# Kernel optimization log

Measured on AMD Instinct MI355X. Metric: run time of the kernel, lower is better.

The kernel has to match this reference:

```python
import jax, jax.numpy as jnp
import numpy as np

N, E, H, D, C, L = 20000, 320000, 8, 64, 512, 2  # nodes, edges, heads, head_dim, channels, layers


def layer_norm(x, g, b, eps=1e-5):
    mu = x.mean(-1, keepdims=True)
    var = ((x - mu) ** 2).mean(-1, keepdims=True)
    return (x - mu) / jnp.sqrt(var + eps) * g + b


def setup_inputs() -> dict:
    key = jax.random.key(0)
    ks = jax.random.split(key, 14)
    s = 0.02
    x = jax.random.normal(ks[0], (N, C), jnp.float32)
    edge_index = jax.random.randint(ks[1], (2, E), 0, N, jnp.int32)
    edge_type = jax.random.randint(ks[2], (E,), 0, 10, jnp.int32)
    edge_repre = jax.random.normal(ks[3], (E,), jnp.float32)
    # Per-layer TransformerConv params (query/key/value/skip linears, each with bias)
    Wq = jax.random.normal(ks[4], (L, C, C), jnp.float32) * s
    Wk = jax.random.normal(ks[5], (L, C, C), jnp.float32) * s
    Wv = jax.random.normal(ks[6], (L, C, C), jnp.float32) * s
    Ws = jax.random.normal(ks[7], (L, C, C), jnp.float32) * s
    bq = jnp.zeros((L, C), jnp.float32)
    bk = jnp.zeros((L, C), jnp.float32)
    bv = jnp.zeros((L, C), jnp.float32)
    bs = jnp.zeros((L, C), jnp.float32)
    # FFN + shared LayerNorm
    W1 = jax.random.normal(ks[8], (C, 2 * C), jnp.float32) * s
    b1 = jnp.zeros((2 * C,), jnp.float32)
    W2 = jax.random.normal(ks[9], (2 * C, C), jnp.float32) * s
    b2 = jnp.zeros((C,), jnp.float32)
    ln_g = jnp.ones((C,), jnp.float32)
    ln_b = jnp.zeros((C,), jnp.float32)
    return {"x": x, "edge_index": edge_index, "edge_type": edge_type, "edge_repre": edge_repre,
            "Wq": Wq, "bq": bq, "Wk": Wk, "bk": bk, "Wv": Wv, "bv": bv, "Ws": Ws, "bs": bs,
            "W1": W1, "b1": b1, "W2": W2, "b2": b2, "ln_g": ln_g, "ln_b": ln_b}


def reference(x, edge_index, edge_type, edge_repre, Wq, bq, Wk, bk, Wv, bv, Ws, bs, W1, b1, W2, b2, ln_g, ln_b):
    src, dst = edge_index[0], edge_index[1]  # messages flow src -> dst (PyG source_to_target)
    enc = x
    scale = 1.0 / jnp.sqrt(jnp.float32(D))
    for l in range(L):
        q = (x @ Wq[l] + bq[l]).reshape(N, H, D)
        k = (x @ Wk[l] + bk[l]).reshape(N, H, D)
        v = (x @ Wv[l] + bv[l]).reshape(N, H, D)
        # per-edge attention logits [E, H]
        a = (q[dst] * k[src]).sum(-1) * scale
        # segment softmax over edges sharing a destination node
        amax = jax.ops.segment_max(a, dst, num_segments=N)
        amax = jnp.where(jnp.isfinite(amax), amax, 0.0)
        e = jnp.exp(a - amax[dst])
        denom = jax.ops.segment_sum(e, dst, num_segments=N)
        alpha = e / (denom[dst] + 1e-16)
        # scatter-aggregate weighted values, concat heads
        agg = jax.ops.segment_sum(alpha[:, :, None] * v[src], dst, num_segments=N).reshape(N, C)
        # root/skip connection (beta=False) + module-level residual to enc_emb
        x = agg + (x @ Ws[l] + bs[l]) + enc
    x = layer_norm(x, ln_g, ln_b)
    x = (jax.nn.relu(x @ W1 + b1) @ W2 + b2) + x
    x = layer_norm(x, ln_g, ln_b)
    return x + enc
```

## Files before the change

### kernel.cpp

```cpp
#include <hip/hip_runtime.h>

typedef __attribute__((ext_vector_type(8))) short short8;
typedef __attribute__((ext_vector_type(4))) float f32x4;

__device__ __forceinline__ unsigned short f2b(float f){
  union { float f; unsigned u; } x; x.f = f;
  unsigned r = x.u + 0x7fffu + ((x.u >> 16) & 1u);
  return (unsigned short)(r >> 16);
}
__device__ __forceinline__ float b2f(unsigned short v){
  union { unsigned u; float f; } x; x.u = ((unsigned)v) << 16; return x.f;
}

__device__ __forceinline__ int pslot(int t){
  return (t & ~7) | ((t & 3) << 1) | ((t >> 2) & 1);
}

__device__ __forceinline__ unsigned char enc1(float v){
#if __has_builtin(__builtin_amdgcn_cvt_pk_fp8_f32)
  return (unsigned char)(__builtin_amdgcn_cvt_pk_fp8_f32(v, v, 0, false) & 0xff);
#else
  union{float f;unsigned u;}x; x.f=v;
  unsigned s = x.u >> 31;
  float av = fabsf(v);
  if (av >= 448.f) return (unsigned char)((s<<7)|0x7e);
  if (av < 0.0078125f){ unsigned d=(unsigned)(av*512.f+0.5f); return (unsigned char)((s<<7)|d); }
  unsigned q = x.u & 0x7fffffff;
  q = q + 0x7ffff + ((q>>20)&1);
  int e2 = (int)(q>>23) - 127;
  unsigned m3 = (q>>20)&7;
  if (e2 < -6){ unsigned d=(unsigned)(av*512.f+0.5f); return (unsigned char)((s<<7)|d); }
  return (unsigned char)((s<<7) | ((unsigned)(e2+7)<<3) | m3);
#endif
}
__device__ __forceinline__ unsigned pk4(float a,float b,float c,float d){
#if __has_builtin(__builtin_amdgcn_cvt_pk_fp8_f32)
  int v = __builtin_amdgcn_cvt_pk_fp8_f32(a, b, 0, false);
  v = __builtin_amdgcn_cvt_pk_fp8_f32(c, d, v, true);
  return (unsigned)v;
#else
  return (unsigned)enc1(a) | ((unsigned)enc1(b)<<8) | ((unsigned)enc1(c)<<16) | ((unsigned)enc1(d)<<24);
#endif
}
__device__ __forceinline__ void dec4(unsigned u, float* o){
#if __has_builtin(__builtin_amdgcn_cvt_pk_f32_fp8)
  auto lo = __builtin_amdgcn_cvt_pk_f32_fp8((int)u, false);
  auto hi = __builtin_amdgcn_cvt_pk_f32_fp8((int)u, true);
  o[0]=lo[0]; o[1]=lo[1]; o[2]=hi[0]; o[3]=hi[1];
#else
  #pragma unroll
  for (int j=0;j<4;j++){
    unsigned b = (u >> (8*j)) & 0xffu;
    unsigned s = b >> 7, ex = (b >> 3) & 15u, mn = b & 7u;
    union{unsigned u;float f;} x;
    x.u = ex ? ((s<<31)|((ex+120u)<<23)|(mn<<20)) : (s<<31);
    o[j] = x.f;
  }
#endif
}

__global__ void count_k(const int* __restrict__ dst, int* __restrict__ deg, int E){
  int e = blockIdx.x*256 + threadIdx.x;
  if (e < E) atomicAdd(&deg[dst[e]], 1);
}

__global__ void scan_k(const int* __restrict__ deg, int* __restrict__ rowstart,
                       int* __restrict__ cursor, int n)
{
  __shared__ int wsum[16];
  int tid = threadIdx.x, lane = tid & 63, wv = tid >> 6;
  int CH = (n + 1023) >> 10;
  int b0 = tid * CH; if (b0 > n) b0 = n;
  int bend = b0 + CH; if (bend > n) bend = n;
  int sum = 0;
  for (int i = b0; i < bend; ++i) sum += deg[i];
  int xs = sum;
  #pragma unroll
  for (int o=1;o<64;o<<=1){ int t = __shfl_up(xs, o, 64); if (lane >= o) xs += t; }
  if (lane == 63) wsum[wv] = xs;
  __syncthreads();
  if (tid < 16){
    int w = wsum[tid];
    #pragma unroll
    for (int o=1;o<16;o<<=1){ int t = __shfl_up(w, o, 64); if (tid >= o) w += t; }
    wsum[tid] = w;
  }
  __syncthreads();
  int off = (wv ? wsum[wv-1] : 0) + xs - sum;
  int run = off;
  for (int i = b0; i < bend; ++i){ rowstart[i] = run; cursor[i] = run; run += deg[i]; }
  if (b0 < n && bend == n) rowstart[n] = run;
  if (n == 0 && tid == 0) rowstart[0] = 0;
}

__global__ void fill_k(const int* __restrict__ src, const int* __restrict__ dst,
                       int* __restrict__ cursor, int* __restrict__ csrc, int E){
  int e = blockIdx.x*256 + threadIdx.x;
  if (e < E){
    int p = atomicAdd(&cursor[dst[e]], 1);
    csrc[p] = src[e];
  }
}

__global__ void transpose_all_k(const float* __restrict__ Wq, const float* __restrict__ Wk,
  const float* __restrict__ Wv, const float* __restrict__ Ws,
  const float* __restrict__ W1, const float* __restrict__ W2,
  unsigned char* __restrict__ wtqkvs8, unsigned char* __restrict__ wt1_8,
  unsigned char* __restrict__ wt2_8)
{
  int bid = blockIdx.x;
  const float* src; unsigned char* dst; int r, c, lb;
  if (bid < 1024){
    int j = bid >> 7;
    int l = j >> 2, w = j & 3;
    src = (w==0?Wq : w==1?Wk : w==2?Wv : Ws) + (size_t)l*512*512;
    dst = wtqkvs8 + ((size_t)l*2048 + (size_t)w*512)*512;
    r = 512; c = 512; lb = bid & 127;
  } else if (bid < 1280){ src = W1; dst = wt1_8; r = 512; c = 1024; lb = bid - 1024; }
  else { src = W2; dst = wt2_8; r = 1024; c = 512; lb = bid - 1280; }
  int idx = lb*256 + threadIdx.x;
  int o = idx % c;
  int i0 = (idx / c) << 3;
  float v[8];
  #pragma unroll
  for (int t=0;t<8;t++) v[t] = 64.f * src[(size_t)(i0+t)*c + o];
  unsigned lo = pk4(v[0],v[1],v[2],v[3]);
  unsigned hi = pk4(v[4],v[5],v[6],v[7]);
  *(unsigned long long*)&dst[(size_t)o*r + pslot(i0>>3)*8] =
      (unsigned long long)lo | ((unsigned long long)hi << 32);
}

__global__ void cvt8_k(const float* __restrict__ in, unsigned char* __restrict__ out8,
                       unsigned short* __restrict__ outb, size_t n){
  size_t i = ((size_t)blockIdx.x*256 + threadIdx.x)*8;
  if (i >= n) return;
  const float4* p = (const float4*)(in + i);
  float4 a0 = p[0], a1 = p[1];
  short8 vv;
  ((unsigned short*)&vv)[0] = f2b(a0.x); ((unsigned short*)&vv)[1] = f2b(a0.y);
  ((unsigned short*)&vv)[2] = f2b(a0.z); ((unsigned short*)&vv)[3] = f2b(a0.w);
  ((unsigned short*)&vv)[4] = f2b(a1.x); ((unsigned short*)&vv)[5] = f2b(a1.y);
  ((unsigned short*)&vv)[6] = f2b(a1.z); ((unsigned short*)&vv)[7] = f2b(a1.w);
  *(short8*)&outb[i] = vv;
  unsigned lo = pk4(a0.x,a0.y,a0.z,a0.w);
  unsigned hi = pk4(a1.x,a1.y,a1.z,a1.w);
  size_t op = (i & ~(size_t)511) | ((size_t)pslot((int)((i & 511) >> 3)) << 3);
  *(unsigned long long*)&out8[op] = (unsigned long long)lo | ((unsigned long long)hi<<32);
}

template<int MODE, int KC, int NN>
__global__ __launch_bounds__(256) void gemm8_k(
    const unsigned char* __restrict__ A8,
    const unsigned char* __restrict__ Bt8,
    int M,
    const float* __restrict__ bias0, const float* __restrict__ bias1,
    const float* __restrict__ bias2, const float* __restrict__ bias3,
    unsigned short* __restrict__ qb, unsigned short* __restrict__ skipb,
    unsigned char* __restrict__ outC,
    float* __restrict__ outF, const float* __restrict__ res)
{
  __shared__ __align__(16) unsigned char lA[128*128];
  __shared__ __align__(16) unsigned char lB[128*128];
  const int tid  = threadIdx.x;
  const int lane = tid & 63;
  const int wid  = tid >> 6;

  const int nwg = gridDim.x;
  int id = blockIdx.x;
  int q = nwg >> 3, r = nwg & 7;
  int xc = id & 7, yy = id >> 3;
  int swz = (xc < r ? xc*(q+1) : r*(q+1) + (xc-r)*q) + yy;
  const int bm = (swz / NN) * 128;
  const int bn = (swz % NN) * 128;
  const int wm = (wid >> 1) * 64;
  const int wn = (wid & 1) * 64;

  f32x4 acc[4][4];
  #pragma unroll
  for (int m=0;m<4;m++)
    #pragma unroll
    for (int n=0;n<4;n++) acc[m][n] = (f32x4)0.f;

  const int kq = lane >> 4;

  for (int kt = 0; kt < KC; kt += 128){
    #pragma unroll
    for (int it = 0; it < 4; ++it) {
      int chunk = it*256 + tid;
      int row = chunk >> 3;
      int cin = chunk & 7;
      int scol = (cin ^ (row & 7)) * 16;
      int ga = bm + row; if (ga >= M) ga = M - 1;
      __builtin_amdgcn_global_load_lds(
        (const __attribute__((address_space(1))) void*)(A8 + (size_t)ga*KC + kt + scol),
        (__attribute__((address_space(3))) void*)(&lA[(it*256 + (wid<<6))*16]),
        16, 0, 0);
      __builtin_amdgcn_global_load_lds(
        (const __attribute__((address_space(1))) void*)(Bt8 + (size_t)(bn + row)*KC + kt + scol),
        (__attribute__((address_space(3))) void*)(&lB[(it*256 + (wid<<6))*16]),
        16, 0, 0);
    }
    __syncthreads();
    #pragma unroll
    for (int S = 0; S < 2; ++S){
      ulonglong2 af[4], bfv[4];
      #pragma unroll
      for (int m=0;m<4;m++){
        int rr = wm + m*16 + (lane & 15);
        int c  = (S*4 + kq) ^ (rr & 7);
        af[m] = *(const ulonglong2*)&lA[rr*128 + c*16];
      }
      #pragma unroll
      for (int n=0;n<4;n++){
        int rr = wn + n*16 + (lane & 15);
        int c  = (S*4 + kq) ^ (rr & 7);
        bfv[n] = *(const ulonglong2*)&lB[rr*128 + c*16];
      }
      #pragma unroll
      for (int m=0;m<4;m++)
        #pragma unroll
        for (int n=0;n<4;n++){
          acc[m][n] = __builtin_amdgcn_mfma_f32_16x16x32_fp8_fp8(
              (long)af[m].x, (long)bfv[n].x, acc[m][n], 0,0,0);
          acc[m][n] = __builtin_amdgcn_mfma_f32_16x16x32_fp8_fp8(
              (long)af[m].y, (long)bfv[n].y, acc[m][n], 0,0,0);
        }
    }
    __syncthreads();
  }

  #pragma unroll
  for (int m=0;m<4;m++){
    int row0 = bm + wm + m*16 + ((lane >> 4) << 2);
    #pragma unroll
    for (int n=0;n<4;n++){
      int col = bn + wn + n*16 + (lane & 15);
      float bval;
      if (MODE == 0){
        bval = (col < 512) ? bias0[col]
             : (col < 1024) ? bias1[col-512]
             : (col < 1536) ? bias2[col-1024] : bias3[col-1536];
      } else {
        bval = bias0[col];
      }
      #pragma unroll
      for (int r4=0;r4<4;r4++){
        int row = row0 + r4;
        if (row < M){
          float v = acc[m][n][r4] * 0.015625f + bval;
          if (MODE == 0){
            if (col < 512)       qb[(size_t)row*512 + col] = f2b(v);
            else if (col < 1536) outC[(size_t)row*1024 + (col-512)] = enc1(v);
            else                 skipb[(size_t)row*512 + (col-1536)] = f2b(v);
          } else if (MODE == 1){
            v = fmaxf(v, 0.0f);
            int pc = (pslot(col >> 3) << 3) | (col & 7);
            outC[(size_t)row*1024 + pc] = enc1(v);
          } else {
            v += res[(size_t)row*512 + col];
            outF[(size_t)row*512 + col] = v;
          }
        }
      }
    }
  }
}

template<int OUT>
__global__ __launch_bounds__(256) void attn_k(
  const unsigned short* __restrict__ qb, const unsigned char* __restrict__ kv8,
  const unsigned short* __restrict__ skipb, const unsigned short* __restrict__ encb,
  const int* __restrict__ rowstart, const int* __restrict__ csrc,
  float* __restrict__ xout, unsigned char* __restrict__ xout8, int N)
{
  int n = blockIdx.x*4 + (threadIdx.x>>6);
  if (n >= N) return;
  int lane = threadIdx.x & 63;

  const short8 qv = *(const short8*)&qb[(size_t)n*512 + lane*8];
  size_t base = (size_t)n*512 + (size_t)lane*8;
  const short8 sv = *(const short8*)&skipb[base];
  const short8 ev = *(const short8*)&encb[base];
  float qf[8];
  #pragma unroll
  for (int j=0;j<8;j++) qf[j] = b2f(((const unsigned short*)&qv)[j]);

  float l = 0.f;
  float acc[8] = {0.f,0.f,0.f,0.f,0.f,0.f,0.f,0.f};
  int e = rowstart[n], e1 = rowstart[n+1];
  if (e < e1){
    int s0 = csrc[e];
    int s1 = (e+1 < e1) ? csrc[e+1] : s0;
    uint2 k0 = *(const uint2*)&kv8[(size_t)s0*1024 + lane*8];
    uint2 v0 = *(const uint2*)&kv8[(size_t)s0*1024 + 512 + lane*8];
    uint2 k1 = *(const uint2*)&kv8[(size_t)s1*1024 + lane*8];
    uint2 v1 = *(const uint2*)&kv8[(size_t)s1*1024 + 512 + lane*8];
    for (; e < e1; ++e){
      int s2 = (e+2 < e1) ? csrc[e+2] : s0;
      uint2 k2 = *(const uint2*)&kv8[(size_t)s2*1024 + lane*8];
      uint2 v2 = *(const uint2*)&kv8[(size_t)s2*1024 + 512 + lane*8];
      float kf[8]; dec4(k0.x, kf); dec4(k0.y, kf+4);
      float dot = 0.f;
      #pragma unroll
      for (int j=0;j<8;j++) dot += qf[j]*kf[j];
      dot += __shfl_xor(dot,1); dot += __shfl_xor(dot,2); dot += __shfl_xor(dot,4);
      float p = __expf(dot * 0.125f);
      l += p;
      float vf[8]; dec4(v0.x, vf); dec4(v0.y, vf+4);
      #pragma unroll
      for (int j=0;j<8;j++) acc[j] += p*vf[j];
      k0 = k1; v0 = v1; k1 = k2; v1 = v2;
    }
  }
  float inv = 1.f/(l + 1e-16f);
  float o[8];
  #pragma unroll
  for (int j=0;j<8;j++)
    o[j] = acc[j]*inv + b2f(((const unsigned short*)&sv)[j]) + b2f(((const unsigned short*)&ev)[j]);
  if (OUT == 0){
    unsigned lo = pk4(o[0],o[1],o[2],o[3]);
    unsigned hi = pk4(o[4],o[5],o[6],o[7]);
    size_t op = (size_t)n*512 + ((size_t)pslot(lane) << 3);
    *(unsigned long long*)&xout8[op] = (unsigned long long)lo | ((unsigned long long)hi<<32);
  } else {
    float4* po = (float4*)&xout[base];
    po[0] = make_float4(o[0],o[1],o[2],o[3]);
    po[1] = make_float4(o[4],o[5],o[6],o[7]);
  }
}

template<int MODE>
__global__ __launch_bounds__(256) void ln_k(const float* __restrict__ x,
  const float* __restrict__ g, const float* __restrict__ b,
  float* __restrict__ outF, unsigned char* __restrict__ out8,
  const float* __restrict__ addv, int N)
{
  int n = blockIdx.x*4 + (threadIdx.x>>6);
  if (n >= N) return;
  int lane = threadIdx.x & 63;
  size_t base = (size_t)n*512 + (size_t)lane*8;
  const float4* p = (const float4*)(x + base);
  float4 a0 = p[0], a1 = p[1];
  float v[8] = {a0.x,a0.y,a0.z,a0.w,a1.x,a1.y,a1.z,a1.w};
  float s=0.f, ss=0.f;
  #pragma unroll
  for (int j=0;j<8;j++){ s += v[j]; ss += v[j]*v[j]; }
  #pragma unroll
  for (int o=1;o<64;o<<=1){ s += __shfl_xor(s,o); ss += __shfl_xor(ss,o); }
  float mean = s * (1.f/512.f);
  float var  = ss * (1.f/512.f) - mean*mean;
  float rstd = rsqrtf(var + 1e-5f);
  float o[8];
  #pragma unroll
  for (int j=0;j<8;j++){
    int c = lane*8 + j;
    o[j] = (v[j]-mean)*rstd*g[c] + b[c];
  }
  if (MODE == 0){
    float4* po = (float4*)&outF[base];
    po[0] = make_float4(o[0],o[1],o[2],o[3]);
    po[1] = make_float4(o[4],o[5],o[6],o[7]);
    unsigned lo = pk4(o[0],o[1],o[2],o[3]);
    unsigned hi = pk4(o[4],o[5],o[6],o[7]);
    size_t op = (size_t)n*512 + ((size_t)pslot(lane) << 3);
    *(unsigned long long*)&out8[op] = (unsigned long long)lo | ((unsigned long long)hi<<32);
  } else {
    #pragma unroll
    for (int j=0;j<8;j++) outF[base+j] = o[j] + addv[base+j];
  }
}

extern "C" void kernel_launch(void* const* d_in, const int* in_sizes, int n_in,
                              void* d_out, int out_size, void* d_ws, size_t ws_size,
                              hipStream_t stream)
{
  const float* x0  = (const float*)d_in[0];
  const int*  eidx = (const int*)d_in[1];
  const float* Wq  = (const float*)d_in[4];
  const float* bq  = (const float*)d_in[5];
  const float* Wk  = (const float*)d_in[6];
  const float* bk  = (const float*)d_in[7];
  const float* Wv  = (const float*)d_in[8];
  const float* bv  = (const float*)d_in[9];
  const float* Wsk = (const float*)d_in[10];
  const float* bs  = (const float*)d_in[11];
  const float* W1  = (const float*)d_in[12];
  const float* b1  = (const float*)d_in[13];
  const float* W2  = (const float*)d_in[14];
  const float* b2  = (const float*)d_in[15];
  const float* lng = (const float*)d_in[16];
  const float* lnb = (const float*)d_in[17];

  const int N = in_sizes[0] / 512;
  const int E = in_sizes[1] / 2;
  const int* esrc = eidx;
  const int* edst = eidx + E;

  char* ws = (char*)d_ws;
  size_t off = 0;
  auto alloc = [&](size_t bytes)->char*{
    char* p = ws + off; off = (off + bytes + 255) & ~(size_t)255; return p;
  };
  unsigned char*  wtqkvs8 = (unsigned char*)alloc((size_t)2*2048*512);
  unsigned char*  wt1_8   = (unsigned char*)alloc((size_t)1024*512);
  unsigned char*  wt2_8   = (unsigned char*)alloc((size_t)512*1024);
  unsigned short* qb      = (unsigned short*)alloc((size_t)N*512*2);
  unsigned char*  kv8     = (unsigned char*)alloc((size_t)N*1024);
  float*          skip    = (float*)alloc((size_t)N*512*4);
  float*          xbuf    = (float*)alloc((size_t)N*512*4);
  unsigned char*  xb8     = (unsigned char*)alloc((size_t)N*512);
  unsigned short* encb    = (unsigned short*)alloc((size_t)N*512*2);
  unsigned short* skipb   = (unsigned short*)alloc((size_t)N*512*2);
  int* deg      = (int*)alloc((size_t)N*4);
  int* rowstart = (int*)alloc((size_t)(N+1)*4);
  int* cursor   = (int*)alloc((size_t)N*4);
  int* csrc     = (int*)alloc((size_t)E*4);
  unsigned char* t8 = (unsigned char*)qb;
  unsigned char* h8 = xb8;

  hipMemsetAsync(deg, 0, (size_t)N*4, stream);
  count_k<<<(E+255)/256, 256, 0, stream>>>(edst, deg, E);
  scan_k<<<1, 1024, 0, stream>>>(deg, rowstart, cursor, N);
  fill_k<<<(E+255)/256, 256, 0, stream>>>(esrc, edst, cursor, csrc, E);

  transpose_all_k<<<1536, 256, 0, stream>>>(Wq, Wk, Wv, Wsk, W1, W2, wtqkvs8, wt1_8, wt2_8);

  const int cvtBlocks = (int)(((size_t)N*512/8 + 255)/256);
  const int rowBlocks = (N + 3)/4;
  const int MB = (N + 127)/128;

  cvt8_k<<<cvtBlocks, 256, 0, stream>>>(x0, xb8, encb, (size_t)N*512);
  for (int l = 0; l < 2; ++l){
    gemm8_k<0,512,16><<<MB*16, 256, 0, stream>>>(xb8, wtqkvs8 + (size_t)l*2048*512, N,
        bq + l*512, bk + l*512, bv + l*512, bs + l*512, qb, skipb, kv8, nullptr, nullptr);
    if (l == 0)
      attn_k<0><<<rowBlocks, 256, 0, stream>>>(qb, kv8, skipb, encb, rowstart, csrc,
          nullptr, xb8, N);
    else
      attn_k<1><<<rowBlocks, 256, 0, stream>>>(qb, kv8, skipb, encb, rowstart, csrc,
          xbuf, nullptr, N);
  }

  ln_k<0><<<rowBlocks, 256, 0, stream>>>(xbuf, lng, lnb, skip, h8, nullptr, N);
  gemm8_k<1,512,8><<<MB*8, 256, 0, stream>>>(h8, wt1_8, N,
      b1, nullptr, nullptr, nullptr, nullptr, nullptr, t8, nullptr, nullptr);
  gemm8_k<2,1024,4><<<MB*4, 256, 0, stream>>>(t8, wt2_8, N,
      b2, nullptr, nullptr, nullptr, nullptr, nullptr, nullptr, xbuf, skip);
  ln_k<1><<<rowBlocks, 256, 0, stream>>>(xbuf, lng, lnb, (float*)d_out, nullptr, x0, N);
}
```

Baseline: 463.2 us.

## Fuse first LayerNorm into attention kernel and enlarge QKV GEMM M-tile

The second-layer attention kernel now computes the row LayerNorm itself and writes both the fp32 normalized activations and the fp8 copy. This removes a separate ln kernel launch and its round trip through global memory. The GEMM gains an MF template parameter, and the QKVS projection uses 256-row tiles so more reuse comes from each B tile. The trade-off is higher register and LDS use (more accumulators per wave), which may reduce occupancy.

```diff
diff --git a/kernel.cpp b/kernel.cpp
--- a/kernel.cpp
+++ b/kernel.cpp
@@ -148,7 +148,7 @@
   *(unsigned long long*)&out8[op] = (unsigned long long)lo | ((unsigned long long)hi<<32);
 }
 
-template<int MODE, int KC, int NN>
+template<int MODE, int KC, int NN, int MF>
 __global__ __launch_bounds__(256) void gemm8_k(
     const unsigned char* __restrict__ A8,
     const unsigned char* __restrict__ Bt8,
@@ -159,7 +159,8 @@
     unsigned char* __restrict__ outC,
     float* __restrict__ outF, const float* __restrict__ res)
 {
-  __shared__ __align__(16) unsigned char lA[128*128];
+  constexpr int BM = MF*32;
+  __shared__ __align__(16) unsigned char lA[BM*128];
   __shared__ __align__(16) unsigned char lB[128*128];
   const int tid  = threadIdx.x;
   const int lane = tid & 63;
@@ -170,14 +171,14 @@
   int q = nwg >> 3, r = nwg & 7;
   int xc = id & 7, yy = id >> 3;
   int swz = (xc < r ? xc*(q+1) : r*(q+1) + (xc-r)*q) + yy;
-  const int bm = (swz / NN) * 128;
+  const int bm = (swz / NN) * BM;
   const int bn = (swz % NN) * 128;
-  const int wm = (wid >> 1) * 64;
+  const int wm = (wid >> 1) * (MF*16);
   const int wn = (wid & 1) * 64;
 
-  f32x4 acc[4][4];
-  #pragma unroll
-  for (int m=0;m<4;m++)
+  f32x4 acc[MF][4];
+  #pragma unroll
+  for (int m=0;m<MF;m++)
     #pragma unroll
     for (int n=0;n<4;n++) acc[m][n] = (f32x4)0.f;
 
@@ -185,7 +186,7 @@
 
   for (int kt = 0; kt < KC; kt += 128){
     #pragma unroll
-    for (int it = 0; it < 4; ++it) {
+    for (int it = 0; it < MF; ++it) {
       int chunk = it*256 + tid;
       int row = chunk >> 3;
       int cin = chunk & 7;
@@ -195,6 +196,13 @@
         (const __attribute__((address_space(1))) void*)(A8 + (size_t)ga*KC + kt + scol),
         (__attribute__((address_space(3))) void*)(&lA[(it*256 + (wid<<6))*16]),
         16, 0, 0);
+    }
+    #pragma unroll
+    for (int it = 0; it < 4; ++it) {
+      int chunk = it*256 + tid;
+      int row = chunk >> 3;
+      int cin = chunk & 7;
+      int scol = (cin ^ (row & 7)) * 16;
       __builtin_amdgcn_global_load_lds(
         (const __attribute__((address_space(1))) void*)(Bt8 + (size_t)(bn + row)*KC + kt + scol),
         (__attribute__((address_space(3))) void*)(&lB[(it*256 + (wid<<6))*16]),
@@ -203,9 +211,9 @@
     __syncthreads();
     #pragma unroll
     for (int S = 0; S < 2; ++S){
-      ulonglong2 af[4], bfv[4];
-      #pragma unroll
-      for (int m=0;m<4;m++){
+      ulonglong2 af[MF], bfv[4];
+      #pragma unroll
+      for (int m=0;m<MF;m++){
         int rr = wm + m*16 + (lane & 15);
         int c  = (S*4 + kq) ^ (rr & 7);
         af[m] = *(const ulonglong2*)&lA[rr*128 + c*16];
@@ -217,7 +225,7 @@
         bfv[n] = *(const ulonglong2*)&lB[rr*128 + c*16];
       }
       #pragma unroll
-      for (int m=0;m<4;m++)
+      for (int m=0;m<MF;m++)
         #pragma unroll
         for (int n=0;n<4;n++){
           acc[m][n] = __builtin_amdgcn_mfma_f32_16x16x32_fp8_fp8(
@@ -230,7 +238,7 @@
   }
 
   #pragma unroll
-  for (int m=0;m<4;m++){
+  for (int m=0;m<MF;m++){
     int row0 = bm + wm + m*16 + ((lane >> 4) << 2);
     #pragma unroll
     for (int n=0;n<4;n++){
@@ -271,7 +279,8 @@
   const unsigned short* __restrict__ qb, const unsigned char* __restrict__ kv8,
   const unsigned short* __restrict__ skipb, const unsigned short* __restrict__ encb,
   const int* __restrict__ rowstart, const int* __restrict__ csrc,
-  float* __restrict__ xout, unsigned char* __restrict__ xout8, int N)
+  float* __restrict__ xout, unsigned char* __restrict__ xout8,
+  const float* __restrict__ lng, const float* __restrict__ lnb, int N)
 {
   int n = blockIdx.x*4 + (threadIdx.x>>6);
   if (n >= N) return;
@@ -317,23 +326,40 @@
   #pragma unroll
   for (int j=0;j<8;j++)
     o[j] = acc[j]*inv + b2f(((const unsigned short*)&sv)[j]) + b2f(((const unsigned short*)&ev)[j]);
+
   if (OUT == 0){
     unsigned lo = pk4(o[0],o[1],o[2],o[3]);
     unsigned hi = pk4(o[4],o[5],o[6],o[7]);
     size_t op = (size_t)n*512 + ((size_t)pslot(lane) << 3);
     *(unsigned long long*)&xout8[op] = (unsigned long long)lo | ((unsigned long long)hi<<32);
   } else {
+    float s=0.f, ss=0.f;
+    #pragma unroll
+    for (int j=0;j<8;j++){ s += o[j]; ss += o[j]*o[j]; }
+    #pragma unroll
+    for (int w=1;w<64;w<<=1){ s += __shfl_xor(s,w); ss += __shfl_xor(ss,w); }
+    float mean = s * (1.f/512.f);
+    float var  = ss * (1.f/512.f) - mean*mean;
+    float rstd = rsqrtf(var + 1e-5f);
+    float h[8];
+    #pragma unroll
+    for (int j=0;j<8;j++){
+      int c = lane*8 + j;
+      h[j] = (o[j]-mean)*rstd*lng[c] + lnb[c];
+    }
     float4* po = (float4*)&xout[base];
-    po[0] = make_float4(o[0],o[1],o[2],o[3]);
-    po[1] = make_float4(o[4],o[5],o[6],o[7]);
-  }
-}
-
-template<int MODE>
+    po[0] = make_float4(h[0],h[1],h[2],h[3]);
+    po[1] = make_float4(h[4],h[5],h[6],h[7]);
+    unsigned lo = pk4(h[0],h[1],h[2],h[3]);
+    unsigned hi = pk4(h[4],h[5],h[6],h[7]);
+    size_t op = (size_t)n*512 + ((size_t)pslot(lane) << 3);
+    *(unsigned long long*)&xout8[op] = (unsigned long long)lo | ((unsigned long long)hi<<32);
+  }
+}
+
 __global__ __launch_bounds__(256) void ln_k(const float* __restrict__ x,
   const float* __restrict__ g, const float* __restrict__ b,
-  float* __restrict__ outF, unsigned char* __restrict__ out8,
-  const float* __restrict__ addv, int N)
+  float* __restrict__ outF, const float* __restrict__ addv, int N)
 {
   int n = blockIdx.x*4 + (threadIdx.x>>6);
   if (n >= N) return;
@@ -350,23 +376,11 @@
   float mean = s * (1.f/512.f);
   float var  = ss * (1.f/512.f) - mean*mean;
   float rstd = rsqrtf(var + 1e-5f);
-  float o[8];
   #pragma unroll
   for (int j=0;j<8;j++){
     int c = lane*8 + j;
-    o[j] = (v[j]-mean)*rstd*g[c] + b[c];
-  }
-  if (MODE == 0){
-    float4* po = (float4*)&outF[base];
-    po[0] = make_float4(o[0],o[1],o[2],o[3]);
-    po[1] = make_float4(o[4],o[5],o[6],o[7]);
-    unsigned lo = pk4(o[0],o[1],o[2],o[3]);
-    unsigned hi = pk4(o[4],o[5],o[6],o[7]);
-    size_t op = (size_t)n*512 + ((size_t)pslot(lane) << 3);
-    *(unsigned long long*)&out8[op] = (unsigned long long)lo | ((unsigned long long)hi<<32);
-  } else {
-    #pragma unroll
-    for (int j=0;j<8;j++) outF[base+j] = o[j] + addv[base+j];
+    float o = (v[j]-mean)*rstd*g[c] + b[c];
+    outF[base+j] = o + addv[base+j];
   }
 }
 
@@ -427,24 +441,24 @@
 
   const int cvtBlocks = (int)(((size_t)N*512/8 + 255)/256);
   const int rowBlocks = (N + 3)/4;
-  const int MB = (N + 127)/128;
+  const int MB  = (N + 127)/128;
+  const int MB2 = (N + 255)/256;
 
   cvt8_k<<<cvtBlocks, 256, 0, stream>>>(x0, xb8, encb, (size_t)N*512);
   for (int l = 0; l < 2; ++l){
-    gemm8_k<0,512,16><<<MB*16, 256, 0, stream>>>(xb8, wtqkvs8 + (size_t)l*2048*512, N,
+    gemm8_k<0,512,16,8><<<MB2*16, 256, 0, stream>>>(xb8, wtqkvs8 + (size_t)l*2048*512, N,
         bq + l*512, bk + l*512, bv + l*512, bs + l*512, qb, skipb, kv8, nullptr, nullptr);
     if (l == 0)
       attn_k<0><<<rowBlocks, 256, 0, stream>>>(qb, kv8, skipb, encb, rowstart, csrc,
-          nullptr, xb8, N);
+          nullptr, xb8, nullptr, nullptr, N);
     else
-      attn_k<1><<<rowBlocks, 256, 0, stream>>>(qb, kv8, skipb, encb, rowstart, csrc,
-          xbuf, nullptr, N);
-  }
-
-  ln_k<0><<<rowBlocks, 256, 0, stream>>>(xbuf, lng, lnb, skip, h8, nullptr, N);
-  gemm8_k<1,512,8><<<MB*8, 256, 0, stream>>>(h8, wt1_8, N,
+      attn_k<2><<<rowBlocks, 256, 0, stream>>>(qb, kv8, skipb, encb, rowstart, csrc,
+          skip, h8, lng, lnb, N);
+  }
+
+  gemm8_k<1,512,8,4><<<MB*8, 256, 0, stream>>>(h8, wt1_8, N,
       b1, nullptr, nullptr, nullptr, nullptr, nullptr, t8, nullptr, nullptr);
-  gemm8_k<2,1024,4><<<MB*4, 256, 0, stream>>>(t8, wt2_8, N,
+  gemm8_k<2,1024,4,4><<<MB*4, 256, 0, stream>>>(t8, wt2_8, N,
       b2, nullptr, nullptr, nullptr, nullptr, nullptr, nullptr, xbuf, skip);
-  ln_k<1><<<rowBlocks, 256, 0, stream>>>(xbuf, lng, lnb, (float*)d_out, nullptr, x0, N);
-}
+  ln_k<<<rowBlocks, 256, 0, stream>>>(xbuf, lng, lnb, (float*)d_out, x0, N);
+}
```

Result: slower. 603.7 us (+30.3%).
